# Kernel optimization log

Hardware: AMD Instinct MI355X
Metric: run time of the kernel (lower is better)

The kernel has to match this reference:

```python
import jax, jax.numpy as jnp
import numpy as np

N = 50000
E = 800000

def setup_inputs() -> dict:
    key = jax.random.key(0)
    ks = jax.random.split(key, 16)
    dims = [35, 64, 256, 512, 256, 64, 16]
    inp = {
        'x': jax.random.normal(ks[0], (N, 35), dtype=jnp.float32),
        'edge_index': jax.random.randint(ks[1], (2, E), 0, N, dtype=jnp.int32),
    }
    for i in range(6):
        fan_in = dims[i]
        inp[f'W{i+1}'] = jax.random.normal(ks[2 + 2 * i], (dims[i], dims[i + 1]), dtype=jnp.float32) / np.float32(np.sqrt(fan_in))
        inp[f'b{i+1}'] = jax.random.normal(ks[3 + 2 * i], (dims[i + 1],), dtype=jnp.float32) * 0.01
    return inp

def _gcn_norm(edge_index):
    # add self loops, then symmetric normalization (GCNConv defaults)
    loops = jnp.arange(N, dtype=edge_index.dtype)
    src = jnp.concatenate([edge_index[0], loops])
    dst = jnp.concatenate([edge_index[1], loops])
    ones = jnp.ones(src.shape[0], dtype=jnp.float32)
    deg = jax.ops.segment_sum(ones, dst, num_segments=N)
    dinv = jnp.where(deg > 0, jax.lax.rsqrt(deg), 0.0)
    norm = dinv[src] * dinv[dst]
    return src, dst, norm

def _gcn_layer(x, W, b, src, dst, norm):
    h = x @ W                                  # [N, out]
    m = h[src] * norm[:, None]                 # [E+N, out] gathered messages
    agg = jax.ops.segment_sum(m, dst, num_segments=N)
    return agg + b

def reference(x, edge_index, W1, b1, W2, b2, W3, b3, W4, b4, W5, b5, W6, b6):
    src, dst, norm = _gcn_norm(edge_index)
    h = jax.nn.relu(_gcn_layer(x, W1, b1, src, dst, norm))
    h = jax.nn.relu(_gcn_layer(h, W2, b2, src, dst, norm))
    h = jax.nn.relu(_gcn_layer(h, W3, b3, src, dst, norm))
    h = jax.nn.relu(_gcn_layer(h, W4, b4, src, dst, norm))
    h = jax.nn.relu(_gcn_layer(h, W5, b5, src, dst, norm))
    return _gcn_layer(h, W6, b6, src, dst, norm)
```

## Files before the change

### kernel.cpp

```cpp
#include <hip/hip_runtime.h>

#define NN 50000
#define NE 800000

typedef __attribute__((ext_vector_type(8))) _Float16 f16x8;
typedef __attribute__((ext_vector_type(16))) float f32x16;
typedef __attribute__((ext_vector_type(4))) _Float16 half4v;

__device__ inline ushort f2h(float f) {
    _Float16 h = (_Float16)f;
    union { _Float16 h; ushort u; } v; v.h = h;
    return v.u;
}
__device__ inline float h2f(ushort u) {
    union { _Float16 h; ushort u; } v; v.u = u;
    return (float)v.h;
}

typedef unsigned int u32_g __attribute__((address_space(1)));
typedef unsigned int u32_l __attribute__((address_space(3)));
__device__ inline void gload16(const ushort* g, ushort* l) {
    __builtin_amdgcn_global_load_lds((const u32_g*)g, (u32_l*)l, 16, 0, 0);
}

template <bool F16>
__device__ inline float4 ldrow(const float* __restrict__ H, size_t idx) {
    if (F16) {
        half4v h = ((const half4v*)H)[idx];
        return make_float4((float)h.x, (float)h.y, (float)h.z, (float)h.w);
    } else {
        return ((const float4*)H)[idx];
    }
}


__global__ __launch_bounds__(256) void zero_int_kernel(int* __restrict__ p, int n) {
    int i = blockIdx.x * 256 + threadIdx.x;
    if (i < n) p[i] = 0;
}

__global__ __launch_bounds__(256) void count_deg_kernel(const int* __restrict__ dst,
                                                        int* __restrict__ deg) {
    int e = blockIdx.x * 256 + threadIdx.x;
    if (e < NE) atomicAdd(&deg[dst[e]], 1);
}

__global__ __launch_bounds__(256) void scan_blocks_kernel(const int* __restrict__ deg,
                                                          int* __restrict__ out,
                                                          int* __restrict__ blk,
                                                          float* __restrict__ dinv, int n) {
    __shared__ int s[256];
    int tid = threadIdx.x;
    int i = blockIdx.x * 256 + tid;
    int v = (i < n) ? deg[i] : 0;
    if (i < n) dinv[i] = rsqrtf((float)(v + 1));
    s[tid] = v;
    __syncthreads();
    for (int off = 1; off < 256; off <<= 1) {
        int t = (tid >= off) ? s[tid - off] : 0;
        __syncthreads();
        s[tid] += t;
        __syncthreads();
    }
    if (i < n) out[i] = s[tid] - v;
    if (tid == 255) blk[blockIdx.x] = s[255];
}

__global__ __launch_bounds__(256) void scan_sums_kernel(int* __restrict__ blk, int nb,
                                                        int* __restrict__ row_ptr, int n) {
    __shared__ int s[256];
    int tid = threadIdx.x;
    int v = (tid < nb) ? blk[tid] : 0;
    s[tid] = v;
    __syncthreads();
    for (int off = 1; off < 256; off <<= 1) {
        int t = (tid >= off) ? s[tid - off] : 0;
        __syncthreads();
        s[tid] += t;
        __syncthreads();
    }
    if (tid < nb) blk[tid] = s[tid] - v;
    if (tid == 255) row_ptr[n] = s[255];
}

__global__ __launch_bounds__(256) void scan_add_kernel(int* __restrict__ row_ptr,
                                                       const int* __restrict__ blk,
                                                       int* __restrict__ cursor, int n) {
    int i = blockIdx.x * 256 + threadIdx.x;
    if (i < n) {
        int r = row_ptr[i] + blk[blockIdx.x];
        row_ptr[i] = r;
        cursor[i] = r;
    }
}

__global__ __launch_bounds__(256) void scatter_kernel(const int* __restrict__ src,
                                                      const int* __restrict__ dst,
                                                      int* __restrict__ cursor,
                                                      int* __restrict__ col_src) {
    int e = blockIdx.x * 256 + threadIdx.x;
    if (e < NE) {
        int d = dst[e];
        int pos = atomicAdd(&cursor[d], 1);
        col_src[pos] = src[e];
    }
}


__global__ __launch_bounds__(256) void split_all_kernel(
    const float* __restrict__ W2, const float* __restrict__ W3,
    const float* __restrict__ W4, const float* __restrict__ W5,
    ushort* __restrict__ W2th, ushort* __restrict__ W3th,
    ushort* __restrict__ W4th, ushort* __restrict__ W5th) {
    int i = blockIdx.x * 256 + threadIdx.x;
    const float* W; ushort* Wth; int K, Nd, idx;
    if (i < 16384) {
        W = W2; Wth = W2th; K = 64; Nd = 256; idx = i;
    } else if (i < 147456) {
        W = W3; Wth = W3th; K = 256; Nd = 512; idx = i - 16384;
    } else if (i < 278528) {
        W = W4; Wth = W4th; K = 512; Nd = 256; idx = i - 147456;
    } else if (i < 294912) {
        W = W5; Wth = W5th; K = 256; Nd = 64; idx = i - 278528;
    } else {
        return;
    }
    int k = idx / Nd, n = idx - k * Nd;
    Wth[(size_t)n * K + k] = f2h(W[idx]);
}


template <int WD, bool BIAS, bool RELU, bool F16O, bool F16IN>
__global__ __launch_bounds__(256) void aggregate_vec_kernel(
    const float* __restrict__ H, const float* __restrict__ dinv,
    const int* __restrict__ row_ptr, const int* __restrict__ col_src,
    const float* __restrict__ bias, float* __restrict__ out,
    ushort* __restrict__ oh) {
    const int GS = WD / 4;
    const int NPB = 256 / GS;
    int v = blockIdx.x * NPB + (threadIdx.x / GS);
    int lg = threadIdx.x & (GS - 1);
    if (v >= NN) return;
    float dv = dinv[v];
    int beg = row_ptr[v], end = row_ptr[v + 1];
    float4 self = ldrow<F16IN>(H, (size_t)v * GS + lg);
    float4 acc = make_float4(0.f, 0.f, 0.f, 0.f);
    for (int cbeg = beg; cbeg < end; cbeg += GS) {
        int cnt = min(GS, end - cbeg);
        int u_l = (lg < cnt) ? col_src[cbeg + lg] : 0;
        float w_l = (lg < cnt) ? dinv[u_l] : 0.0f;
        int e = 0;
        for (; e + 8 <= cnt; e += 8) {
            int u[8]; float w[8]; float4 h[8];
#pragma unroll
            for (int t = 0; t < 8; ++t) {
                u[t] = __shfl(u_l, e + t, GS);
                w[t] = __shfl(w_l, e + t, GS);
            }
#pragma unroll
            for (int t = 0; t < 8; ++t) h[t] = ldrow<F16IN>(H, (size_t)u[t] * GS + lg);
#pragma unroll
            for (int t = 0; t < 8; ++t) {
                acc.x = fmaf(w[t], h[t].x, acc.x); acc.y = fmaf(w[t], h[t].y, acc.y);
                acc.z = fmaf(w[t], h[t].z, acc.z); acc.w = fmaf(w[t], h[t].w, acc.w);
            }
        }
        for (; e + 4 <= cnt; e += 4) {
            int u[4]; float w[4]; float4 h[4];
#pragma unroll
            for (int t = 0; t < 4; ++t) {
                u[t] = __shfl(u_l, e + t, GS);
                w[t] = __shfl(w_l, e + t, GS);
            }
#pragma unroll
            for (int t = 0; t < 4; ++t) h[t] = ldrow<F16IN>(H, (size_t)u[t] * GS + lg);
#pragma unroll
            for (int t = 0; t < 4; ++t) {
                acc.x = fmaf(w[t], h[t].x, acc.x); acc.y = fmaf(w[t], h[t].y, acc.y);
                acc.z = fmaf(w[t], h[t].z, acc.z); acc.w = fmaf(w[t], h[t].w, acc.w);
            }
        }
        for (; e < cnt; ++e) {
            int u = __shfl(u_l, e, GS);
            float w = __shfl(w_l, e, GS);
            float4 h = ldrow<F16IN>(H, (size_t)u * GS + lg);
            acc.x = fmaf(w, h.x, acc.x); acc.y = fmaf(w, h.y, acc.y);
            acc.z = fmaf(w, h.z, acc.z); acc.w = fmaf(w, h.w, acc.w);
        }
    }
    float dv2 = dv * dv;
    float4 r;
    r.x = fmaf(dv, acc.x, dv2 * self.x);
    r.y = fmaf(dv, acc.y, dv2 * self.y);
    r.z = fmaf(dv, acc.z, dv2 * self.z);
    r.w = fmaf(dv, acc.w, dv2 * self.w);
    if (BIAS) {
        float4 b = ((const float4*)bias)[lg];
        r.x += b.x; r.y += b.y; r.z += b.z; r.w += b.w;
    }
    if (RELU) {
        r.x = fmaxf(r.x, 0.f); r.y = fmaxf(r.y, 0.f);
        r.z = fmaxf(r.z, 0.f); r.w = fmaxf(r.w, 0.f);
    }
    if (F16O) {
        ushort4 hv;
        hv.x = f2h(r.x); hv.y = f2h(r.y); hv.z = f2h(r.z); hv.w = f2h(r.w);
        *(ushort4*)&oh[(size_t)v * WD + lg * 4] = hv;
    } else {
        ((float4*)out)[(size_t)v * GS + lg] = r;
    }
}


template <bool F16OUT, bool BR>
__global__ __launch_bounds__(256, 4) void gemm_f16_kernel(
    const ushort* __restrict__ A, const ushort* __restrict__ Bw,
    const float* __restrict__ bias,
    float* __restrict__ Cf, ushort* __restrict__ Ch,
    int M, int K, int Nd) {
    __shared__ ushort At[2][128][32];
    __shared__ ushort Bt[2][128][32];
    int tid = threadIdx.x;

    int nwg = gridDim.x * gridDim.y;
    int id = blockIdx.y * gridDim.x + blockIdx.x;
    int q = nwg >> 3, r8 = nwg & 7;
    int c = id & 7, s = id >> 3;
    int logical = (c < r8) ? c * (q + 1) + s : r8 * (q + 1) + (c - r8) * q + s;
    int bx = logical % gridDim.x, by = logical / gridDim.x;
    int bm = by * 128, bn = bx * 128;

    int lane = tid & 63;
    int wave = tid >> 6;
    int l31 = lane & 31, q2 = lane >> 5;
    int wm = (wave & 1) * 64, wn = (wave >> 1) * 64;

    int r4 = lane >> 2;
    int c8 = (lane & 3) * 8;

    f32x16 acc[2][2];
#pragma unroll
    for (int i = 0; i < 2; ++i)
#pragma unroll
        for (int j = 0; j < 2; ++j)
#pragma unroll
            for (int r = 0; r < 16; ++r) acc[i][j][r] = 0.0f;

    int arow0 = bm + wave * 32 + r4;       if (arow0 >= M) arow0 = M - 1;
    int arow1 = bm + wave * 32 + 16 + r4;  if (arow1 >= M) arow1 = M - 1;
    int brow0 = bn + wave * 32 + r4;       if (brow0 >= Nd) brow0 = Nd - 1;
    int brow1 = bn + wave * 32 + 16 + r4;  if (brow1 >= Nd) brow1 = Nd - 1;
    const ushort* Ap0 = A + (size_t)arow0 * K + c8;
    const ushort* Ap1 = A + (size_t)arow1 * K + c8;
    const ushort* Bp0 = Bw + (size_t)brow0 * K + c8;
    const ushort* Bp1 = Bw + (size_t)brow1 * K + c8;

    auto stage = [&](int buf, int k0) {
        gload16(Ap0 + k0, &At[buf][wave * 32][0]);
        gload16(Ap1 + k0, &At[buf][wave * 32 + 16][0]);
        gload16(Bp0 + k0, &Bt[buf][wave * 32][0]);
        gload16(Bp1 + k0, &Bt[buf][wave * 32 + 16][0]);
    };

    stage(0, 0);
    int buf = 0;
    for (int k0 = 0; k0 < K; k0 += 32, buf ^= 1) {
        __syncthreads();
        if (k0 + 32 < K) stage(buf ^ 1, k0 + 32);

        f16x8 af[2][2];
#pragma unroll
        for (int i = 0; i < 2; ++i) {
            const ushort* ar = &At[buf][wm + i * 32 + l31][0];
            af[i][0] = *(const f16x8*)(ar + q2 * 8);
            af[i][1] = *(const f16x8*)(ar + 16 + q2 * 8);
        }
#pragma unroll
        for (int j = 0; j < 2; ++j) {
            const ushort* br = &Bt[buf][wn + j * 32 + l31][0];
            f16x8 b0 = *(const f16x8*)(br + q2 * 8);
            f16x8 b1 = *(const f16x8*)(br + 16 + q2 * 8);
#pragma unroll
            for (int i = 0; i < 2; ++i) {
                acc[i][j] = __builtin_amdgcn_mfma_f32_32x32x16_f16(af[i][0], b0, acc[i][j], 0, 0, 0);
                acc[i][j] = __builtin_amdgcn_mfma_f32_32x32x16_f16(af[i][1], b1, acc[i][j], 0, 0, 0);
            }
        }
    }

#pragma unroll
    for (int j = 0; j < 2; ++j) {
        int n = bn + wn + j * 32 + l31;
        if (n >= Nd) continue;
        float bv = BR ? bias[n] : 0.0f;
#pragma unroll
        for (int i = 0; i < 2; ++i) {
            int mb = bm + wm + i * 32 + 4 * q2;
#pragma unroll
            for (int r = 0; r < 16; ++r) {
                int m = mb + (r & 3) + 8 * (r >> 2);
                if (m >= M) continue;
                float v = acc[i][j][r];
                if (BR) v = fmaxf(v + bv, 0.0f);
                if (F16OUT) {
                    Ch[(size_t)m * Nd + n] = f2h(v);
                } else {
                    Cf[(size_t)m * Nd + n] = v;
                }
            }
        }
    }
}


template <bool BIASRELU, bool F16IN, bool F16OUT>
__global__ __launch_bounds__(256, 4) void gemm_small_kernel(
    const float* __restrict__ A, const float* __restrict__ W,
    const float* __restrict__ bias, float* __restrict__ C,
    ushort* __restrict__ Ch,
    int M, int K, int Nd) {
    const int BK = 16;
    __shared__ float As[BK][68];
    __shared__ float Ws[BK][68];
    int bm = blockIdx.y * 64;
    int bn = blockIdx.x * 64;
    int tid = threadIdx.x;
    int tx = tid & 15;
    int ty = tid >> 4;

    int ar = tid >> 2;
    int ac = (tid & 3) * 4;
    int wcol = tid & 63;
    int wk0 = (tid >> 6) * 4;

    float acc[4][4];
#pragma unroll
    for (int i = 0; i < 4; ++i)
#pragma unroll
        for (int j = 0; j < 4; ++j) acc[i][j] = 0.0f;

    for (int k0 = 0; k0 < K; k0 += BK) {
        int gm = bm + ar;
        float a0 = 0.f, a1 = 0.f, a2 = 0.f, a3 = 0.f;
        if (gm < M) {
            int gk = k0 + ac;
            if (F16IN) {
                const ushort* ap = (const ushort*)A + (size_t)gm * K;
                a0 = (gk + 0 < K) ? h2f(ap[gk + 0]) : 0.f;
                a1 = (gk + 1 < K) ? h2f(ap[gk + 1]) : 0.f;
                a2 = (gk + 2 < K) ? h2f(ap[gk + 2]) : 0.f;
                a3 = (gk + 3 < K) ? h2f(ap[gk + 3]) : 0.f;
            } else {
                const float* ap = &A[(size_t)gm * K];
                a0 = (gk + 0 < K) ? ap[gk + 0] : 0.f;
                a1 = (gk + 1 < K) ? ap[gk + 1] : 0.f;
                a2 = (gk + 2 < K) ? ap[gk + 2] : 0.f;
                a3 = (gk + 3 < K) ? ap[gk + 3] : 0.f;
            }
        }
        float w0 = 0.f, w1 = 0.f, w2 = 0.f, w3 = 0.f;
        if (bn + wcol < Nd) {
            int gk = k0 + wk0;
            w0 = (gk + 0 < K) ? W[(size_t)(gk + 0) * Nd + bn + wcol] : 0.f;
            w1 = (gk + 1 < K) ? W[(size_t)(gk + 1) * Nd + bn + wcol] : 0.f;
            w2 = (gk + 2 < K) ? W[(size_t)(gk + 2) * Nd + bn + wcol] : 0.f;
            w3 = (gk + 3 < K) ? W[(size_t)(gk + 3) * Nd + bn + wcol] : 0.f;
        }
        __syncthreads();
        As[ac + 0][ar] = a0;
        As[ac + 1][ar] = a1;
        As[ac + 2][ar] = a2;
        As[ac + 3][ar] = a3;
        Ws[wk0 + 0][wcol] = w0;
        Ws[wk0 + 1][wcol] = w1;
        Ws[wk0 + 2][wcol] = w2;
        Ws[wk0 + 3][wcol] = w3;
        __syncthreads();
#pragma unroll
        for (int kk = 0; kk < BK; ++kk) {
            float4 a = *(const float4*)&As[kk][ty * 4];
            float4 b = *(const float4*)&Ws[kk][tx * 4];
            float af[4] = {a.x, a.y, a.z, a.w};
            float bf[4] = {b.x, b.y, b.z, b.w};
#pragma unroll
            for (int i = 0; i < 4; ++i)
#pragma unroll
                for (int j = 0; j < 4; ++j) acc[i][j] = fmaf(af[i], bf[j], acc[i][j]);
        }
    }

    int col = bn + tx * 4;
    if (col >= Nd) return;
    float4 bi = make_float4(0.f, 0.f, 0.f, 0.f);
    if (BIASRELU) bi = *(const float4*)&bias[col];
#pragma unroll
    for (int i = 0; i < 4; ++i) {
        int m = bm + ty * 4 + i;
        if (m >= M) continue;
        float4 r = make_float4(acc[i][0], acc[i][1], acc[i][2], acc[i][3]);
        if (BIASRELU) {
            r.x = fmaxf(r.x + bi.x, 0.f); r.y = fmaxf(r.y + bi.y, 0.f);
            r.z = fmaxf(r.z + bi.z, 0.f); r.w = fmaxf(r.w + bi.w, 0.f);
        }
        if (F16OUT) {
            ushort4 hv;
            hv.x = f2h(r.x); hv.y = f2h(r.y); hv.z = f2h(r.z); hv.w = f2h(r.w);
            *(ushort4*)&Ch[(size_t)m * Nd + col] = hv;
        } else {
            *(float4*)&C[(size_t)m * Nd + col] = r;
        }
    }
}


extern "C" void kernel_launch(void* const* d_in, const int* in_sizes, int n_in,
                              void* d_out, int out_size, void* d_ws, size_t ws_size,
                              hipStream_t stream) {
    const float* x = (const float*)d_in[0];
    const int* ei = (const int*)d_in[1];
    const int* e_src = ei;
    const int* e_dst = ei + NE;
    const float* W1 = (const float*)d_in[2];
    const float* b1 = (const float*)d_in[3];
    const float* W2 = (const float*)d_in[4];
    const float* b2 = (const float*)d_in[5];
    const float* W3 = (const float*)d_in[6];
    const float* b3 = (const float*)d_in[7];
    const float* W4 = (const float*)d_in[8];
    const float* b4 = (const float*)d_in[9];
    const float* W5 = (const float*)d_in[10];
    const float* b5 = (const float*)d_in[11];
    const float* W6 = (const float*)d_in[12];
    const float* b6 = (const float*)d_in[13];
    float* out = (float*)d_out;

    char* p = (char*)d_ws;
    auto take = [&p](size_t nbytes) {
        char* q = p;
        p += (nbytes + 255) & ~(size_t)255;
        return q;
    };
    char* RA = take((size_t)NN * 1024);
    char* RB = take((size_t)NN * 1024);
    char* RC = take((size_t)NN * 2048);
    float* dinv = (float*)take((size_t)NN * 4);
    int* deg = (int*)take((size_t)NN * 4);
    int* row_ptr = (int*)take((size_t)(NN + 1) * 4);
    int* cursor = (int*)take((size_t)NN * 4);
    int* col_src = (int*)take((size_t)NE * 4);
    int* blk = (int*)take(256 * 4);
    ushort* W2th = (ushort*)take((size_t)64 * 256 * 2);
    ushort* W3th = (ushort*)take((size_t)256 * 512 * 2);
    ushort* W4th = (ushort*)take((size_t)512 * 256 * 2);
    ushort* W5th = (ushort*)take((size_t)256 * 64 * 2);

    ushort* H1h = (ushort*)RA;
    ushort* X1h = (ushort*)RB;
    ushort* A2h = (ushort*)RC;
    ushort* X2h = (ushort*)RA;
    ushort* A3h = (ushort*)RB;
    ushort* X3h = (ushort*)RC;
    ushort* H4h = (ushort*)RA;
    ushort* X4h = (ushort*)RB;
    ushort* H5h = (ushort*)RA;
    ushort* X5h = (ushort*)RB;
    float* H6f = (float*)RA;

    const int nblkN = (NN + 255) / 256;
    const int nblkE = (NE + 255) / 256;

    zero_int_kernel<<<nblkN, 256, 0, stream>>>(deg, NN);
    count_deg_kernel<<<nblkE, 256, 0, stream>>>(e_dst, deg);
    scan_blocks_kernel<<<nblkN, 256, 0, stream>>>(deg, row_ptr, blk, dinv, NN);
    scan_sums_kernel<<<1, 256, 0, stream>>>(blk, nblkN, row_ptr, NN);
    scan_add_kernel<<<nblkN, 256, 0, stream>>>(row_ptr, blk, cursor, NN);
    scatter_kernel<<<nblkE, 256, 0, stream>>>(e_src, e_dst, cursor, col_src);

    split_all_kernel<<<(294912 + 255) / 256, 256, 0, stream>>>(
        W2, W3, W4, W5, W2th, W3th, W4th, W5th);

    const int aggGrid256 = (NN + 3) / 4;
    const int aggGrid64v = (NN + 15) / 16;
    const int aggGrid16v = (NN + 63) / 64;
    const int mrows = (NN + 127) / 128;

    {
        dim3 g(1, (NN + 63) / 64);
        gemm_small_kernel<false, false, true><<<g, 256, 0, stream>>>(
            x, W1, nullptr, nullptr, H1h, NN, 35, 64);
    }
    aggregate_vec_kernel<64, true, true, true, true><<<aggGrid64v, 256, 0, stream>>>(
        (const float*)H1h, dinv, row_ptr, col_src, b1, nullptr, X1h);
    aggregate_vec_kernel<64, false, false, true, true><<<aggGrid64v, 256, 0, stream>>>(
        (const float*)X1h, dinv, row_ptr, col_src, nullptr, nullptr, A2h);
    {
        dim3 g(2, mrows);
        gemm_f16_kernel<true, true><<<g, 256, 0, stream>>>(A2h, W2th, b2,
                                                           nullptr, X2h, NN, 64, 256);
    }
    aggregate_vec_kernel<256, false, false, true, true><<<aggGrid256, 256, 0, stream>>>(
        (const float*)X2h, dinv, row_ptr, col_src, nullptr, nullptr, A3h);
    {
        dim3 g(4, mrows);
        gemm_f16_kernel<true, true><<<g, 256, 0, stream>>>(A3h, W3th, b3,
                                                           nullptr, X3h, NN, 256, 512);
    }
    {
        dim3 g(2, mrows);
        gemm_f16_kernel<true, false><<<g, 256, 0, stream>>>(X3h, W4th, nullptr,
                                                            nullptr, H4h, NN, 512, 256);
    }
    aggregate_vec_kernel<256, true, true, true, true><<<aggGrid256, 256, 0, stream>>>(
        (const float*)H4h, dinv, row_ptr, col_src, b4, nullptr, X4h);
    {
        dim3 g(1, mrows);
        gemm_f16_kernel<true, false><<<g, 256, 0, stream>>>(X4h, W5th, nullptr,
                                                            nullptr, H5h, NN, 256, 64);
    }
    aggregate_vec_kernel<64, true, true, true, true><<<aggGrid64v, 256, 0, stream>>>(
        (const float*)H5h, dinv, row_ptr, col_src, b5, nullptr, X5h);
    {
        dim3 g(1, (NN + 63) / 64);
        gemm_small_kernel<false, true, false><<<g, 256, 0, stream>>>(
            (const float*)X5h, W6, nullptr, H6f, nullptr, NN, 64, 16);
    }
    aggregate_vec_kernel<16, true, false, false, false><<<aggGrid16v, 256, 0, stream>>>(
        H6f, dinv, row_ptr, col_src, b6, out, nullptr);
}
```

Before: 494.3 us.

## Split sparse aggregation passes into two column halves for gather locality

The aggregation kernel gets a total-row-width template parameter and a column offset, so each sparse aggregation runs as two launches that each handle half of the feature columns. The idea is to halve the width of the gathered feature rows per pass, shrinking the randomly accessed working set so more of it stays cached. In exchange, the CSR indices and degree scalings are read twice, more launches are issued, and smaller thread groups spend more shuffles per edge.

```diff
diff --git a/kernel.cpp b/kernel.cpp
--- a/kernel.cpp
+++ b/kernel.cpp
@@ -130,20 +130,21 @@
 }
 
 
-template <int WD, bool BIAS, bool RELU, bool F16O, bool F16IN>
+template <int WD, int WDT, bool BIAS, bool RELU, bool F16O, bool F16IN>
 __global__ __launch_bounds__(256) void aggregate_vec_kernel(
     const float* __restrict__ H, const float* __restrict__ dinv,
     const int* __restrict__ row_ptr, const int* __restrict__ col_src,
     const float* __restrict__ bias, float* __restrict__ out,
-    ushort* __restrict__ oh) {
+    ushort* __restrict__ oh, int goff) {
     const int GS = WD / 4;
+    const int RG = WDT / 4;
     const int NPB = 256 / GS;
     int v = blockIdx.x * NPB + (threadIdx.x / GS);
     int lg = threadIdx.x & (GS - 1);
     if (v >= NN) return;
     float dv = dinv[v];
     int beg = row_ptr[v], end = row_ptr[v + 1];
-    float4 self = ldrow<F16IN>(H, (size_t)v * GS + lg);
+    float4 self = ldrow<F16IN>(H, (size_t)v * RG + goff + lg);
     float4 acc = make_float4(0.f, 0.f, 0.f, 0.f);
     for (int cbeg = beg; cbeg < end; cbeg += GS) {
         int cnt = min(GS, end - cbeg);
@@ -158,7 +159,7 @@
                 w[t] = __shfl(w_l, e + t, GS);
             }
 #pragma unroll
-            for (int t = 0; t < 8; ++t) h[t] = ldrow<F16IN>(H, (size_t)u[t] * GS + lg);
+            for (int t = 0; t < 8; ++t) h[t] = ldrow<F16IN>(H, (size_t)u[t] * RG + goff + lg);
 #pragma unroll
             for (int t = 0; t < 8; ++t) {
                 acc.x = fmaf(w[t], h[t].x, acc.x); acc.y = fmaf(w[t], h[t].y, acc.y);
@@ -173,7 +174,7 @@
                 w[t] = __shfl(w_l, e + t, GS);
             }
 #pragma unroll
-            for (int t = 0; t < 4; ++t) h[t] = ldrow<F16IN>(H, (size_t)u[t] * GS + lg);
+            for (int t = 0; t < 4; ++t) h[t] = ldrow<F16IN>(H, (size_t)u[t] * RG + goff + lg);
 #pragma unroll
             for (int t = 0; t < 4; ++t) {
                 acc.x = fmaf(w[t], h[t].x, acc.x); acc.y = fmaf(w[t], h[t].y, acc.y);
@@ -183,7 +184,7 @@
         for (; e < cnt; ++e) {
             int u = __shfl(u_l, e, GS);
             float w = __shfl(w_l, e, GS);
-            float4 h = ldrow<F16IN>(H, (size_t)u * GS + lg);
+            float4 h = ldrow<F16IN>(H, (size_t)u * RG + goff + lg);
             acc.x = fmaf(w, h.x, acc.x); acc.y = fmaf(w, h.y, acc.y);
             acc.z = fmaf(w, h.z, acc.z); acc.w = fmaf(w, h.w, acc.w);
         }
@@ -195,7 +196,7 @@
     r.z = fmaf(dv, acc.z, dv2 * self.z);
     r.w = fmaf(dv, acc.w, dv2 * self.w);
     if (BIAS) {
-        float4 b = ((const float4*)bias)[lg];
+        float4 b = ((const float4*)bias)[goff + lg];
         r.x += b.x; r.y += b.y; r.z += b.z; r.w += b.w;
     }
     if (RELU) {
@@ -205,9 +206,9 @@
     if (F16O) {
         ushort4 hv;
         hv.x = f2h(r.x); hv.y = f2h(r.y); hv.z = f2h(r.z); hv.w = f2h(r.w);
-        *(ushort4*)&oh[(size_t)v * WD + lg * 4] = hv;
+        *(ushort4*)&oh[(size_t)v * WDT + (goff + lg) * 4] = hv;
     } else {
-        ((float4*)out)[(size_t)v * GS + lg] = r;
+        ((float4*)out)[(size_t)v * RG + goff + lg] = r;
     }
 }
 
@@ -479,8 +480,8 @@
     split_all_kernel<<<(294912 + 255) / 256, 256, 0, stream>>>(
         W2, W3, W4, W5, W2th, W3th, W4th, W5th);
 
-    const int aggGrid256 = (NN + 3) / 4;
-    const int aggGrid64v = (NN + 15) / 16;
+    const int aggGrid128 = (NN + 7) / 8;
+    const int aggGrid32 = (NN + 31) / 32;
     const int aggGrid16v = (NN + 63) / 64;
     const int mrows = (NN + 127) / 128;
 
@@ -489,17 +490,23 @@
         gemm_small_kernel<false, false, true><<<g, 256, 0, stream>>>(
             x, W1, nullptr, nullptr, H1h, NN, 35, 64);
     }
-    aggregate_vec_kernel<64, true, true, true, true><<<aggGrid64v, 256, 0, stream>>>(
-        (const float*)H1h, dinv, row_ptr, col_src, b1, nullptr, X1h);
-    aggregate_vec_kernel<64, false, false, true, true><<<aggGrid64v, 256, 0, stream>>>(
-        (const float*)X1h, dinv, row_ptr, col_src, nullptr, nullptr, A2h);
+    aggregate_vec_kernel<32, 64, true, true, true, true><<<aggGrid32, 256, 0, stream>>>(
+        (const float*)H1h, dinv, row_ptr, col_src, b1, nullptr, X1h, 0);
+    aggregate_vec_kernel<32, 64, true, true, true, true><<<aggGrid32, 256, 0, stream>>>(
+        (const float*)H1h, dinv, row_ptr, col_src, b1, nullptr, X1h, 8);
+    aggregate_vec_kernel<32, 64, false, false, true, true><<<aggGrid32, 256, 0, stream>>>(
+        (const float*)X1h, dinv, row_ptr, col_src, nullptr, nullptr, A2h, 0);
+    aggregate_vec_kernel<32, 64, false, false, true, true><<<aggGrid32, 256, 0, stream>>>(
+        (const float*)X1h, dinv, row_ptr, col_src, nullptr, nullptr, A2h, 8);
     {
         dim3 g(2, mrows);
         gemm_f16_kernel<true, true><<<g, 256, 0, stream>>>(A2h, W2th, b2,
                                                            nullptr, X2h, NN, 64, 256);
     }
-    aggregate_vec_kernel<256, false, false, true, true><<<aggGrid256, 256, 0, stream>>>(
-        (const float*)X2h, dinv, row_ptr, col_src, nullptr, nullptr, A3h);
+    aggregate_vec_kernel<128, 256, false, false, true, true><<<aggGrid128, 256, 0, stream>>>(
+        (const float*)X2h, dinv, row_ptr, col_src, nullptr, nullptr, A3h, 0);
+    aggregate_vec_kernel<128, 256, false, false, true, true><<<aggGrid128, 256, 0, stream>>>(
+        (const float*)X2h, dinv, row_ptr, col_src, nullptr, nullptr, A3h, 32);
     {
         dim3 g(4, mrows);
         gemm_f16_kernel<true, true><<<g, 256, 0, stream>>>(A3h, W3th, b3,
@@ -510,20 +517,24 @@
         gemm_f16_kernel<true, false><<<g, 256, 0, stream>>>(X3h, W4th, nullptr,
                                                             nullptr, H4h, NN, 512, 256);
     }
-    aggregate_vec_kernel<256, true, true, true, true><<<aggGrid256, 256, 0, stream>>>(
-        (const float*)H4h, dinv, row_ptr, col_src, b4, nullptr, X4h);
+    aggregate_vec_kernel<128, 256, true, true, true, true><<<aggGrid128, 256, 0, stream>>>(
+        (const float*)H4h, dinv, row_ptr, col_src, b4, nullptr, X4h, 0);
+    aggregate_vec_kernel<128, 256, true, true, true, true><<<aggGrid128, 256, 0, stream>>>(
+        (const float*)H4h, dinv, row_ptr, col_src, b4, nullptr, X4h, 32);
     {
         dim3 g(1, mrows);
         gemm_f16_kernel<true, false><<<g, 256, 0, stream>>>(X4h, W5th, nullptr,
                                                             nullptr, H5h, NN, 256, 64);
     }
-    aggregate_vec_kernel<64, true, true, true, true><<<aggGrid64v, 256, 0, stream>>>(
-        (const float*)H5h, dinv, row_ptr, col_src, b5, nullptr, X5h);
+    aggregate_vec_kernel<32, 64, true, true, true, true><<<aggGrid32, 256, 0, stream>>>(
+        (const float*)H5h, dinv, row_ptr, col_src, b5, nullptr, X5h, 0);
+    aggregate_vec_kernel<32, 64, true, true, true, true><<<aggGrid32, 256, 0, stream>>>(
+        (const float*)H5h, dinv, row_ptr, col_src, b5, nullptr, X5h, 8);
     {
         dim3 g(1, (NN + 63) / 64);
         gemm_small_kernel<false, true, false><<<g, 256, 0, stream>>>(
             (const float*)X5h, W6, nullptr, H6f, nullptr, NN, 64, 16);
     }
-    aggregate_vec_kernel<16, true, false, false, false><<<aggGrid16v, 256, 0, stream>>>(
-        H6f, dinv, row_ptr, col_src, b6, out, nullptr);
-}
+    aggregate_vec_kernel<16, 16, true, false, false, false><<<aggGrid16v, 256, 0, stream>>>(
+        H6f, dinv, row_ptr, col_src, b6, out, nullptr, 0);
+}
```

New measurement: 538.9 us. +9.0%, slower.

## Replace atomic CSR build with two-level LDS bucket sort by destination

Applied to the files above, without the earlier changes.

Builds the CSR adjacency with a bucketed counting sort instead of per-edge global atomics. Edges are first binned into 256-node buckets through shared-memory histograms and staging, then each bucket is sorted locally in LDS, which also yields row_ptr and dinv. This cuts global atomic contention and the number of launches in preprocessing, and makes per-row edge order deterministic. The cost is an extra edge buffer, and it relies on each bucket holding at most BCAP edges, which could overflow on skewed graphs.

```diff
diff --git a/kernel.cpp b/kernel.cpp
--- a/kernel.cpp
+++ b/kernel.cpp
@@ -2,6 +2,9 @@
 
 #define NN 50000
 #define NE 800000
+#define NBUK 196
+#define EB_BLOCKS 196
+#define BCAP 5120
 
 typedef __attribute__((ext_vector_type(8))) _Float16 f16x8;
 typedef __attribute__((ext_vector_type(16))) float f32x16;
@@ -39,71 +42,143 @@
     if (i < n) p[i] = 0;
 }
 
-__global__ __launch_bounds__(256) void count_deg_kernel(const int* __restrict__ dst,
-                                                        int* __restrict__ deg) {
-    int e = blockIdx.x * 256 + threadIdx.x;
-    if (e < NE) atomicAdd(&deg[dst[e]], 1);
-}
-
-__global__ __launch_bounds__(256) void scan_blocks_kernel(const int* __restrict__ deg,
-                                                          int* __restrict__ out,
-                                                          int* __restrict__ blk,
-                                                          float* __restrict__ dinv, int n) {
+__global__ __launch_bounds__(256) void bucket_hist_kernel(const int* __restrict__ dst,
+                                                          int* __restrict__ gcnt) {
+    __shared__ int cnt[256];
+    int tid = threadIdx.x;
+    cnt[tid] = 0;
+    __syncthreads();
+    int e0 = blockIdx.x * 4096;
+#pragma unroll
+    for (int i = 0; i < 16; ++i) {
+        int e = e0 + i * 256 + tid;
+        if (e < NE) atomicAdd(&cnt[dst[e] >> 8], 1);
+    }
+    __syncthreads();
+    if (tid < NBUK && cnt[tid] > 0) atomicAdd(&gcnt[tid], cnt[tid]);
+}
+
+__global__ __launch_bounds__(256) void bucket_scan_kernel(const int* __restrict__ gcnt,
+                                                          int* __restrict__ bbase,
+                                                          int* __restrict__ bcur,
+                                                          int* __restrict__ row_ptr) {
     __shared__ int s[256];
     int tid = threadIdx.x;
-    int i = blockIdx.x * 256 + tid;
-    int v = (i < n) ? deg[i] : 0;
-    if (i < n) dinv[i] = rsqrtf((float)(v + 1));
+    int v = (tid < NBUK) ? gcnt[tid] : 0;
     s[tid] = v;
     __syncthreads();
-    for (int off = 1; off < 256; off <<= 1) {
-        int t = (tid >= off) ? s[tid - off] : 0;
+    for (int o = 1; o < 256; o <<= 1) {
+        int t = (tid >= o) ? s[tid - o] : 0;
         __syncthreads();
         s[tid] += t;
         __syncthreads();
     }
-    if (i < n) out[i] = s[tid] - v;
-    if (tid == 255) blk[blockIdx.x] = s[255];
-}
-
-__global__ __launch_bounds__(256) void scan_sums_kernel(int* __restrict__ blk, int nb,
-                                                        int* __restrict__ row_ptr, int n) {
-    __shared__ int s[256];
+    int excl = s[tid] - v;
+    if (tid < NBUK) { bbase[tid] = excl; bcur[tid] = excl; }
+    if (tid == 0) row_ptr[NN] = NE;
+}
+
+__global__ __launch_bounds__(256) void edge_bin_kernel(const int* __restrict__ src,
+                                                       const int* __restrict__ dst,
+                                                       int* __restrict__ bcur,
+                                                       unsigned* __restrict__ ebuf) {
+    __shared__ int cnt[256];
+    __shared__ int off[256];
+    __shared__ int cur[256];
+    __shared__ int gbase[256];
+    __shared__ unsigned stage[4096];
+    __shared__ unsigned char bmap[4096];
     int tid = threadIdx.x;
-    int v = (tid < nb) ? blk[tid] : 0;
-    s[tid] = v;
-    __syncthreads();
-    for (int off = 1; off < 256; off <<= 1) {
-        int t = (tid >= off) ? s[tid - off] : 0;
-        __syncthreads();
-        s[tid] += t;
-        __syncthreads();
-    }
-    if (tid < nb) blk[tid] = s[tid] - v;
-    if (tid == 255) row_ptr[n] = s[255];
-}
-
-__global__ __launch_bounds__(256) void scan_add_kernel(int* __restrict__ row_ptr,
-                                                       const int* __restrict__ blk,
-                                                       int* __restrict__ cursor, int n) {
-    int i = blockIdx.x * 256 + threadIdx.x;
-    if (i < n) {
-        int r = row_ptr[i] + blk[blockIdx.x];
-        row_ptr[i] = r;
-        cursor[i] = r;
-    }
-}
-
-__global__ __launch_bounds__(256) void scatter_kernel(const int* __restrict__ src,
-                                                      const int* __restrict__ dst,
-                                                      int* __restrict__ cursor,
-                                                      int* __restrict__ col_src) {
-    int e = blockIdx.x * 256 + threadIdx.x;
-    if (e < NE) {
-        int d = dst[e];
-        int pos = atomicAdd(&cursor[d], 1);
-        col_src[pos] = src[e];
-    }
+    int e0 = blockIdx.x * 4096;
+    int filled = min(4096, NE - e0);
+    cnt[tid] = 0;
+    __syncthreads();
+#pragma unroll
+    for (int i = 0; i < 16; ++i) {
+        int e = e0 + i * 256 + tid;
+        if (e < NE) atomicAdd(&cnt[dst[e] >> 8], 1);
+    }
+    __syncthreads();
+    int v = cnt[tid];
+    off[tid] = v;
+    __syncthreads();
+    for (int o = 1; o < 256; o <<= 1) {
+        int t = (tid >= o) ? off[tid - o] : 0;
+        __syncthreads();
+        off[tid] += t;
+        __syncthreads();
+    }
+    int excl = off[tid] - v;
+    __syncthreads();
+    off[tid] = excl;
+    cur[tid] = excl;
+    if (tid < NBUK && v > 0) gbase[tid] = atomicAdd(&bcur[tid], v);
+    __syncthreads();
+#pragma unroll
+    for (int i = 0; i < 16; ++i) {
+        int e = e0 + i * 256 + tid;
+        if (e < NE) {
+            int d = dst[e];
+            int b = d >> 8;
+            int p = atomicAdd(&cur[b], 1);
+            stage[p] = ((unsigned)src[e] << 8) | (unsigned)(d & 255);
+            bmap[p] = (unsigned char)b;
+        }
+    }
+    __syncthreads();
+    for (int s2 = tid; s2 < filled; s2 += 256) {
+        int b = bmap[s2];
+        ebuf[gbase[b] + (s2 - off[b])] = stage[s2];
+    }
+}
+
+__global__ __launch_bounds__(256) void bucket_sort_kernel(const int* __restrict__ bbase,
+                                                          const unsigned* __restrict__ ebuf,
+                                                          int* __restrict__ col_src,
+                                                          int* __restrict__ row_ptr,
+                                                          float* __restrict__ dinv) {
+    __shared__ int cnt[256];
+    __shared__ int off[256];
+    __shared__ int cur[256];
+    __shared__ unsigned pk[BCAP];
+    __shared__ int outv[BCAP];
+    int tid = threadIdx.x;
+    int nb = blockIdx.x;
+    int n0 = nb << 8;
+    int base = bbase[nb];
+    int cntE = ((nb + 1 < NBUK) ? bbase[nb + 1] : NE) - base;
+    cnt[tid] = 0;
+    __syncthreads();
+    for (int e = tid; e < cntE; e += 256) {
+        unsigned p = ebuf[base + e];
+        pk[e] = p;
+        atomicAdd(&cnt[(int)(p & 255u)], 1);
+    }
+    __syncthreads();
+    int v = cnt[tid];
+    off[tid] = v;
+    __syncthreads();
+    for (int o = 1; o < 256; o <<= 1) {
+        int t = (tid >= o) ? off[tid - o] : 0;
+        __syncthreads();
+        off[tid] += t;
+        __syncthreads();
+    }
+    int excl = off[tid] - v;
+    cur[tid] = excl;
+    int n = n0 + tid;
+    if (n < NN) {
+        row_ptr[n] = base + excl;
+        dinv[n] = rsqrtf((float)(v + 1));
+    }
+    __syncthreads();
+    for (int e = tid; e < cntE; e += 256) {
+        unsigned p = pk[e];
+        int pos = atomicAdd(&cur[(int)(p & 255u)], 1);
+        outv[pos] = (int)(p >> 8);
+    }
+    __syncthreads();
+    for (int e = tid; e < cntE; e += 256) col_src[base + e] = outv[e];
 }
 
 
@@ -444,11 +519,12 @@
     char* RB = take((size_t)NN * 1024);
     char* RC = take((size_t)NN * 2048);
     float* dinv = (float*)take((size_t)NN * 4);
-    int* deg = (int*)take((size_t)NN * 4);
     int* row_ptr = (int*)take((size_t)(NN + 1) * 4);
-    int* cursor = (int*)take((size_t)NN * 4);
     int* col_src = (int*)take((size_t)NE * 4);
-    int* blk = (int*)take(256 * 4);
+    unsigned* ebuf = (unsigned*)take((size_t)NE * 4);
+    int* gcnt = (int*)take(256 * 4);
+    int* bbase = (int*)take(256 * 4);
+    int* bcur = (int*)take(256 * 4);
     ushort* W2th = (ushort*)take((size_t)64 * 256 * 2);
     ushort* W3th = (ushort*)take((size_t)256 * 512 * 2);
     ushort* W4th = (ushort*)take((size_t)512 * 256 * 2);
@@ -466,15 +542,11 @@
     ushort* X5h = (ushort*)RB;
     float* H6f = (float*)RA;
 
-    const int nblkN = (NN + 255) / 256;
-    const int nblkE = (NE + 255) / 256;
-
-    zero_int_kernel<<<nblkN, 256, 0, stream>>>(deg, NN);
-    count_deg_kernel<<<nblkE, 256, 0, stream>>>(e_dst, deg);
-    scan_blocks_kernel<<<nblkN, 256, 0, stream>>>(deg, row_ptr, blk, dinv, NN);
-    scan_sums_kernel<<<1, 256, 0, stream>>>(blk, nblkN, row_ptr, NN);
-    scan_add_kernel<<<nblkN, 256, 0, stream>>>(row_ptr, blk, cursor, NN);
-    scatter_kernel<<<nblkE, 256, 0, stream>>>(e_src, e_dst, cursor, col_src);
+    zero_int_kernel<<<1, 256, 0, stream>>>(gcnt, 256);
+    bucket_hist_kernel<<<EB_BLOCKS, 256, 0, stream>>>(e_dst, gcnt);
+    bucket_scan_kernel<<<1, 256, 0, stream>>>(gcnt, bbase, bcur, row_ptr);
+    edge_bin_kernel<<<EB_BLOCKS, 256, 0, stream>>>(e_src, e_dst, bcur, ebuf);
+    bucket_sort_kernel<<<NBUK, 256, 0, stream>>>(bbase, ebuf, col_src, row_ptr, dinv);
 
     split_all_kernel<<<(294912 + 255) / 256, 256, 0, stream>>>(
         W2, W3, W4, W5, W2th, W3th, W4th, W5th);
```

After: 434.0 us. 1.14x faster.
